# Kernel optimization log

Hardware: AMD Instinct MI355X
Metric: run time of the kernel (lower is better)

The kernel has to match this reference:

```python
import jax, jax.numpy as jnp
import numpy as np

# Faithful JAX port of predictTransform: YOLO anchor-box decode.
# prediction: [B, A*(5+C), G, G] raw conv output.
# Returns [B, G*G*A, 5+C] decoded boxes in input-image pixel units.

def setup_inputs() -> dict:
    key = jax.random.key(0)
    B, A, C, IN_DIM, G = 32, 3, 80, 608, 76  # stride = 608 // 76 = 8
    attrs = 5 + C
    prediction = jax.random.normal(key, (B, A * attrs, G, G), dtype=jnp.float32)
    # standard YOLOv3 anchors for the stride-8 head, in input-pixel units
    anchors = jnp.array([[10.0, 13.0], [16.0, 30.0], [33.0, 23.0]], dtype=jnp.float32)
    return {"prediction": prediction, "anchors": anchors, "inputDim": IN_DIM, "numClasses": C}


def reference(prediction, anchors, inputDim, numClasses):
    B = prediction.shape[0]
    stride = inputDim // prediction.shape[2]
    G = inputDim // stride
    A = anchors.shape[0]
    attrs = 5 + numClasses

    # [B, A*attrs, G*G] -> [B, G*G, A*attrs] -> [B, G*G*A, attrs]
    p = prediction.reshape(B, attrs * A, G * G)
    p = jnp.transpose(p, (0, 2, 1)).reshape(B, G * G * A, attrs)

    anc = anchors / stride  # anchors in grid units, [A, 2]

    # grid offsets: np.meshgrid(grid, grid) -> a[i,j]=j (x), b[i,j]=i (y)
    grid = jnp.arange(G, dtype=jnp.float32)
    gx, gy = jnp.meshgrid(grid, grid)  # each [G, G]
    xy = jnp.stack([gx.ravel(), gy.ravel()], axis=-1)        # [G*G, 2]
    xy = jnp.repeat(xy, A, axis=0)[None]                     # [1, G*G*A, 2]
    anc_t = jnp.tile(anc, (G * G, 1))[None]                  # [1, G*G*A, 2]

    txy = jax.nn.sigmoid(p[..., 0:2]) + xy                   # center x,y in grid units
    twh = jnp.exp(p[..., 2:4]) * anc_t                       # w,h in grid units
    conf = jax.nn.sigmoid(p[..., 4:5])                       # objectness
    cls = jax.nn.sigmoid(p[..., 5:])                         # class probs

    boxes = jnp.concatenate([txy, twh], axis=-1) * stride    # back to pixel units
    return jnp.concatenate([boxes, conf, cls], axis=-1)
```

## Files before the change

### kernel.cpp

```cpp
#include <hip/hip_runtime.h>


#define BATCH   32
#define ATTRS   85
#define CH      255
#define GRID    76
#define SP      5776
#define STRIDE_F 8.0f
#define S_TILE  32
#define TPB     1024
#define TILES_PER_B 181
#define NTILES  (BATCH * TILES_PER_B)
#define NBLK    512
#define NF4     (CH * (S_TILE / 4))

typedef float f4 __attribute__((ext_vector_type(4)));

__device__ __forceinline__ float decode1(float val, int attr, int s,
                                         float ax, float ay) {
    if (attr == 2) return __expf(val) * ax;
    if (attr == 3) return __expf(val) * ay;
    const float sg = __builtin_amdgcn_rcpf(1.0f + __expf(-val));
    if (attr == 0) return (sg + (float)(s % GRID)) * STRIDE_F;
    if (attr == 1) return (sg + (float)(s / GRID)) * STRIDE_F;
    return sg;
}

__global__ __launch_bounds__(TPB, 8) void yolo_decode_kernel(
        const float* __restrict__ pred,
        const float* __restrict__ anchors,
        float* __restrict__ out) {
    __shared__ float buf[2][S_TILE * CH];

    const int tid = threadIdx.x;

    const float a0x = anchors[0], a0y = anchors[1];
    const float a1x = anchors[2], a1y = anchors[3];
    const float a2x = anchors[4], a2y = anchors[5];

    const int c0  = tid >> 3;
    const int sl0 = (tid & 7) * 4;
    const int j1  = tid + TPB;
    const int c1  = j1 >> 3;
    const int sl1 = (j1 & 7) * 4;
    const bool have1 = (j1 < NF4);

    const int aI0 = c0 / ATTRS, attr0 = c0 - aI0 * ATTRS;
    const int aI1 = c1 / ATTRS, attr1 = c1 - aI1 * ATTRS;
    const float ax0 = (aI0 == 0) ? a0x : (aI0 == 1) ? a1x : a2x;
    const float ay0 = (aI0 == 0) ? a0y : (aI0 == 1) ? a1y : a2y;
    const float ax1 = (aI1 == 0) ? a0x : (aI1 == 1) ? a1x : a2x;
    const float ay1 = (aI1 == 0) ? a0y : (aI1 == 1) ? a1y : a2y;

    int tk = blockIdx.x;
    int b  = tk / TILES_PER_B;
    int t  = tk - b * TILES_PER_B;
    int s0 = t * S_TILE;
    int sw = (t == TILES_PER_B - 1) ? (SP - s0) : S_TILE;
    const float* src = pred + (size_t)b * ((size_t)CH * SP) + s0;

    f4 v0 = {0.f, 0.f, 0.f, 0.f}, v1 = {0.f, 0.f, 0.f, 0.f};
    if (sl0 < sw)          v0 = *(const f4*)(src + (size_t)c0 * SP + sl0);
    if (have1 && sl1 < sw) v1 = *(const f4*)(src + (size_t)c1 * SP + sl1);

    int it = 0;
    for (;;) {
        float* __restrict__ B = buf[it & 1];
        const int cb = b, cs0 = s0, csw = sw;

        #pragma unroll
        for (int e = 0; e < 4; ++e)
            B[(sl0 + e) * CH + c0] = decode1(v0[e], attr0, cs0 + sl0 + e, ax0, ay0);
        if (have1) {
            #pragma unroll
            for (int e = 0; e < 4; ++e)
                B[(sl1 + e) * CH + c1] = decode1(v1[e], attr1, cs0 + sl1 + e, ax1, ay1);
        }

        const int ntk = tk + NBLK;
        const bool more = (ntk < NTILES);
        if (more) {
            b  = ntk / TILES_PER_B;
            t  = ntk - b * TILES_PER_B;
            s0 = t * S_TILE;
            sw = (t == TILES_PER_B - 1) ? (SP - s0) : S_TILE;
            src = pred + (size_t)b * ((size_t)CH * SP) + s0;
            if (sl0 < sw)          v0 = *(const f4*)(src + (size_t)c0 * SP + sl0);
            if (have1 && sl1 < sw) v1 = *(const f4*)(src + (size_t)c1 * SP + sl1);
        }

        __syncthreads();

        const float* __restrict__ Bs = buf[it & 1];
        float* __restrict__ dst = out + (size_t)cb * ((size_t)SP * CH)
                                      + (size_t)cs0 * CH;
        const int nf4w = (csw * CH) >> 2;
        for (int j = tid; j < nf4w; j += TPB) {
            f4 w = *(const f4*)(Bs + j * 4);
            __builtin_nontemporal_store(w, (f4*)(dst + j * 4));
        }

        if (!more) break;
        tk = ntk;
        ++it;
    }
}

extern "C" void kernel_launch(void* const* d_in, const int* in_sizes, int n_in,
                              void* d_out, int out_size, void* d_ws, size_t ws_size,
                              hipStream_t stream) {
    const float* pred    = (const float*)d_in[0];
    const float* anchors = (const float*)d_in[1];
    float* out = (float*)d_out;

    yolo_decode_kernel<<<NBLK, TPB, 0, stream>>>(pred, anchors, out);
}
```

Baseline: 76.05 us.

## Double spatial tile, single LDS buffer, and custom barriers with four loads per thread

Raises the spatial tile from 32 to 64 positions and remaps threads so each handles four channels (stride 64) over a 4-wide spatial vector. The double LDS buffer becomes a single buffer protected by two hand-placed barriers per iteration, and the first barrier waits only on LDS counters so the prefetch global loads stay in flight across it. The goal is more bytes in flight per iteration and fewer loop trips. In exchange there is an extra barrier per iteration, the LDS footprint per block grows, and the last tile is uneven.

```diff
diff --git a/kernel.cpp b/kernel.cpp
--- a/kernel.cpp
+++ b/kernel.cpp
@@ -4,15 +4,14 @@
 #define BATCH   32
 #define ATTRS   85
 #define CH      255
-#define GRID    76
+#define G_      76
 #define SP      5776
 #define STRIDE_F 8.0f
-#define S_TILE  32
+#define S_TILE  64
 #define TPB     1024
-#define TILES_PER_B 181
+#define TILES_PER_B 91
 #define NTILES  (BATCH * TILES_PER_B)
 #define NBLK    512
-#define NF4     (CH * (S_TILE / 4))
 
 typedef float f4 __attribute__((ext_vector_type(4)));
 
@@ -21,8 +20,8 @@
     if (attr == 2) return __expf(val) * ax;
     if (attr == 3) return __expf(val) * ay;
     const float sg = __builtin_amdgcn_rcpf(1.0f + __expf(-val));
-    if (attr == 0) return (sg + (float)(s % GRID)) * STRIDE_F;
-    if (attr == 1) return (sg + (float)(s / GRID)) * STRIDE_F;
+    if (attr == 0) return (sg + (float)(s % G_)) * STRIDE_F;
+    if (attr == 1) return (sg + (float)(s / G_)) * STRIDE_F;
     return sg;
 }
 
@@ -30,7 +29,7 @@
         const float* __restrict__ pred,
         const float* __restrict__ anchors,
         float* __restrict__ out) {
-    __shared__ float buf[2][S_TILE * CH];
+    __shared__ float lds[S_TILE * CH];
 
     const int tid = threadIdx.x;
 
@@ -38,43 +37,50 @@
     const float a1x = anchors[2], a1y = anchors[3];
     const float a2x = anchors[4], a2y = anchors[5];
 
-    const int c0  = tid >> 3;
-    const int sl0 = (tid & 7) * 4;
-    const int j1  = tid + TPB;
-    const int c1  = j1 >> 3;
-    const int sl1 = (j1 & 7) * 4;
-    const bool have1 = (j1 < NF4);
+    const int c0 = ((tid >> 6) << 2) | (tid & 3);
+    const int sl = ((tid >> 2) & 15) << 2;
+    const bool act3 = (c0 + 192) < CH;
 
-    const int aI0 = c0 / ATTRS, attr0 = c0 - aI0 * ATTRS;
-    const int aI1 = c1 / ATTRS, attr1 = c1 - aI1 * ATTRS;
-    const float ax0 = (aI0 == 0) ? a0x : (aI0 == 1) ? a1x : a2x;
-    const float ay0 = (aI0 == 0) ? a0y : (aI0 == 1) ? a1y : a2y;
-    const float ax1 = (aI1 == 0) ? a0x : (aI1 == 1) ? a1x : a2x;
-    const float ay1 = (aI1 == 0) ? a0y : (aI1 == 1) ? a1y : a2y;
+    const int cA = c0,       aA = cA / ATTRS, atA = cA - aA * ATTRS;
+    const int cB = c0 + 64,  aB = cB / ATTRS, atB = cB - aB * ATTRS;
+    const int cC = c0 + 128, aC = cC / ATTRS, atC = cC - aC * ATTRS;
+    const int cD = c0 + 192, aD = cD / ATTRS, atD = cD - aD * ATTRS;
+    const float axA = (aA == 0) ? a0x : (aA == 1) ? a1x : a2x;
+    const float ayA = (aA == 0) ? a0y : (aA == 1) ? a1y : a2y;
+    const float axB = (aB == 0) ? a0x : (aB == 1) ? a1x : a2x;
+    const float ayB = (aB == 0) ? a0y : (aB == 1) ? a1y : a2y;
+    const float axC = (aC == 0) ? a0x : (aC == 1) ? a1x : a2x;
+    const float ayC = (aC == 0) ? a0y : (aC == 1) ? a1y : a2y;
+    const float axD = (aD == 0) ? a0x : (aD == 1) ? a1x : a2x;
+    const float ayD = (aD == 0) ? a0y : (aD == 1) ? a1y : a2y;
 
     int tk = blockIdx.x;
     int b  = tk / TILES_PER_B;
     int t  = tk - b * TILES_PER_B;
     int s0 = t * S_TILE;
     int sw = (t == TILES_PER_B - 1) ? (SP - s0) : S_TILE;
-    const float* src = pred + (size_t)b * ((size_t)CH * SP) + s0;
+    const float* src = pred + (size_t)b * ((size_t)CH * SP) + s0 + sl;
 
-    f4 v0 = {0.f, 0.f, 0.f, 0.f}, v1 = {0.f, 0.f, 0.f, 0.f};
-    if (sl0 < sw)          v0 = *(const f4*)(src + (size_t)c0 * SP + sl0);
-    if (have1 && sl1 < sw) v1 = *(const f4*)(src + (size_t)c1 * SP + sl1);
+    f4 v0 = {0,0,0,0}, v1 = {0,0,0,0}, v2 = {0,0,0,0}, v3 = {0,0,0,0};
+    if (sl < sw) {
+        v0 = *(const f4*)(src + (size_t)cA * SP);
+        v1 = *(const f4*)(src + (size_t)cB * SP);
+        v2 = *(const f4*)(src + (size_t)cC * SP);
+        if (act3) v3 = *(const f4*)(src + (size_t)cD * SP);
+    }
 
-    int it = 0;
     for (;;) {
-        float* __restrict__ B = buf[it & 1];
         const int cb = b, cs0 = s0, csw = sw;
 
-        #pragma unroll
-        for (int e = 0; e < 4; ++e)
-            B[(sl0 + e) * CH + c0] = decode1(v0[e], attr0, cs0 + sl0 + e, ax0, ay0);
-        if (have1) {
+        if (sl < csw) {
             #pragma unroll
-            for (int e = 0; e < 4; ++e)
-                B[(sl1 + e) * CH + c1] = decode1(v1[e], attr1, cs0 + sl1 + e, ax1, ay1);
+            for (int e = 0; e < 4; ++e) {
+                const int r = sl + e, s = cs0 + r;
+                lds[r * CH + cA] = decode1(v0[e], atA, s, axA, ayA);
+                lds[r * CH + cB] = decode1(v1[e], atB, s, axB, ayB);
+                lds[r * CH + cC] = decode1(v2[e], atC, s, axC, ayC);
+                if (act3) lds[r * CH + cD] = decode1(v3[e], atD, s, axD, ayD);
+            }
         }
 
         const int ntk = tk + NBLK;
@@ -84,25 +90,36 @@
             t  = ntk - b * TILES_PER_B;
             s0 = t * S_TILE;
             sw = (t == TILES_PER_B - 1) ? (SP - s0) : S_TILE;
-            src = pred + (size_t)b * ((size_t)CH * SP) + s0;
-            if (sl0 < sw)          v0 = *(const f4*)(src + (size_t)c0 * SP + sl0);
-            if (have1 && sl1 < sw) v1 = *(const f4*)(src + (size_t)c1 * SP + sl1);
+            src = pred + (size_t)b * ((size_t)CH * SP) + s0 + sl;
+            if (sl < sw) {
+                v0 = *(const f4*)(src + (size_t)cA * SP);
+                v1 = *(const f4*)(src + (size_t)cB * SP);
+                v2 = *(const f4*)(src + (size_t)cC * SP);
+                if (act3) v3 = *(const f4*)(src + (size_t)cD * SP);
+            }
         }
 
-        __syncthreads();
+        asm volatile("s_waitcnt lgkmcnt(0)" ::: "memory");
+        __builtin_amdgcn_sched_barrier(0);
+        __builtin_amdgcn_s_barrier();
+        __builtin_amdgcn_sched_barrier(0);
 
-        const float* __restrict__ Bs = buf[it & 1];
         float* __restrict__ dst = out + (size_t)cb * ((size_t)SP * CH)
                                       + (size_t)cs0 * CH;
         const int nf4w = (csw * CH) >> 2;
         for (int j = tid; j < nf4w; j += TPB) {
-            f4 w = *(const f4*)(Bs + j * 4);
-            __builtin_nontemporal_store(w, (f4*)(dst + j * 4));
+            f4 w = *(const f4*)(lds + 4 * j);
+            __builtin_nontemporal_store(w, (f4*)(dst + 4 * j));
         }
 
         if (!more) break;
+
+        asm volatile("" ::: "memory");
+        __builtin_amdgcn_sched_barrier(0);
+        __builtin_amdgcn_s_barrier();
+        __builtin_amdgcn_sched_barrier(0);
+
         tk = ntk;
-        ++it;
     }
 }
 
```

Result: faster. 73.15 us (-3.8%).
